# Kernel tuning notes

Measured on AMD Instinct MI355X. Metric: run time of the kernel, lower is better.

Reference implementation:

```python
import jax, jax.numpy as jnp
import numpy as np

N = 100000      # nodes
E = 3200000     # edges (avg degree 32)
F_IN = 500      # input features
HID = 8         # per-head hidden dim (layer 1)
HEADS = 8       # heads (layer 1)
NC = 41         # num classes (layer 2, 1 head)


def setup_inputs() -> dict:
    key = jax.random.key(0)
    ks = jax.random.split(key, 8)
    x = jax.random.normal(ks[0], (N, F_IN), jnp.float32)
    edge_index = jax.random.randint(ks[1], (2, E), 0, N, dtype=jnp.int64)
    W1 = jax.random.normal(ks[2], (F_IN, HEADS * HID), jnp.float32) / np.sqrt(F_IN)
    a1_src = jax.random.normal(ks[3], (HEADS, HID), jnp.float32) / np.sqrt(HID)
    a1_dst = jax.random.normal(ks[4], (HEADS, HID), jnp.float32) / np.sqrt(HID)
    W2 = jax.random.normal(ks[5], (HEADS * HID, NC), jnp.float32) / np.sqrt(HEADS * HID)
    a2_src = jax.random.normal(ks[6], (1, NC), jnp.float32) / np.sqrt(NC)
    a2_dst = jax.random.normal(ks[7], (1, NC), jnp.float32) / np.sqrt(NC)
    return {"x": x, "edge_index": edge_index, "W1": W1, "a1_src": a1_src,
            "a1_dst": a1_dst, "W2": W2, "a2_src": a2_src, "a2_dst": a2_dst}


def gat_layer(x, edge_index, W, a_src, a_dst, heads, out_dim, concat):
    n = x.shape[0]
    h = (x @ W).reshape(n, heads, out_dim)                    # [N,H,D]
    # per-node attention halves (avoids gathering full features for logits)
    alpha_src = jnp.einsum('nhd,hd->nh', h, a_src)            # [N,H]
    alpha_dst = jnp.einsum('nhd,hd->nh', h, a_dst)            # [N,H]
    src, dst = edge_index[0], edge_index[1]
    e = jax.nn.leaky_relu(alpha_src[src] + alpha_dst[dst], 0.2)  # [E,H]
    # segment softmax over incoming edges of each destination node
    e_max = jax.lax.stop_gradient(jax.ops.segment_max(e, dst, num_segments=n))
    e_exp = jnp.exp(e - e_max[dst])
    denom = jax.ops.segment_sum(e_exp, dst, num_segments=n)
    alpha = e_exp / (denom[dst] + 1e-16)                      # [E,H]
    msg = alpha[:, :, None] * h[src]                          # [E,H,D]
    out = jax.ops.segment_sum(msg, dst, num_segments=n)       # [N,H,D]
    return out.reshape(n, heads * out_dim) if concat else out.mean(axis=1)


def reference(x, edge_index, W1, a1_src, a1_dst, W2, a2_src, a2_dst):
    # dropout layers are identity at inference
    h = gat_layer(x, edge_index, W1, a1_src, a1_dst, HEADS, HID, True)   # [N,64]
    h = jax.nn.elu(h)
    out = gat_layer(h, edge_index, W2, a2_src, a2_dst, 1, NC, False)     # [N,41]
    return jax.nn.log_softmax(out, axis=1)
```

## Files before the change

kernel.cpp:

```cpp
#include <hip/hip_runtime.h>
#include <hip/hip_bf16.h>
#include <math.h>


#define DEV __device__ __forceinline__

constexpr int N_NODES = 100000;
constexpr int N_EDGES = 3200000;
constexpr int F_IN    = 500;
constexpr int HEADS   = 8;
constexpr int HID     = 8;
constexpr int D1      = HEADS * HID;
constexpr int NC      = 41;

constexpr int NB    = 196;
constexpr int BCAP  = 20480;
constexpr int SEPT  = 16;
constexpr int SCHUNK = 256 * SEPT;

constexpr int GROWS = 32;
constexpr int LROW  = 520;

constexpr int WSTR = 68;

typedef __attribute__((ext_vector_type(8))) short bf16x8;
typedef __attribute__((ext_vector_type(4))) float f32x4;

DEV float bf2f(unsigned short u) {
    return __uint_as_float(((unsigned int)u) << 16);
}
DEV unsigned short f2b(float f) {
    unsigned int u = __float_as_uint(f);
    unsigned int r = (u + 0x7FFFu + ((u >> 16) & 1u)) >> 16;
    return (unsigned short)r;
}
DEV float leaky(float e) { return e > 0.f ? e : 0.2f * e; }
DEV float readlane_f(float v, int l) {
    return __uint_as_float((unsigned int)__builtin_amdgcn_readlane((int)__float_as_uint(v), l));
}

__global__ void k_detect(const void* xraw, const void* eraw, int* flags) {
    const int lane = threadIdx.x & 63;
    const unsigned short* xu = (const unsigned short*)xraw;
    unsigned short v = xu[2 * lane];
    int e = (v >> 7) & 0xFF;
    int valid = (e == 0 || (e >= 90 && e <= 150)) ? 1 : 0;
    unsigned long long vm = __ballot(valid);
    const unsigned int* eu = (const unsigned int*)eraw;
    unsigned long long zm = __ballot(eu[2 * lane + 1] == 0u);
    if (lane == 0) {
        flags[0] = (__popcll(vm) < 56) ? 1 : 0;
        flags[1] = (__popcll(zm) == 64) ? 1 : 0;
    }
}

__global__ __launch_bounds__(256) void k_convert(const void* w1, const void* a1s, const void* a1d,
                                                 const void* w2, const void* a2s, const void* a2d,
                                                 const int* flags,
                                                 unsigned short* W1frag, float* A1Sf, float* A1Df,
                                                 float* W2f, float* A2Sf, float* A2Df) {
    const bool f32 = flags[0] != 0;
    if (blockIdx.x == 0) {
        auto conv = [&](const void* src, float* dst, int n) {
            if (f32) {
                const float* s = (const float*)src;
                for (int i = threadIdx.x; i < n; i += blockDim.x) dst[i] = s[i];
            } else {
                const unsigned short* s = (const unsigned short*)src;
                for (int i = threadIdx.x; i < n; i += blockDim.x) dst[i] = bf2f(s[i]);
            }
        };
        conv(a1s, A1Sf, HEADS * HID);
        conv(a1d, A1Df, HEADS * HID);
        conv(w2, W2f, D1 * NC);
        conv(a2s, A2Sf, NC);
        conv(a2d, A2Df, NC);
    }
    for (int idx = blockIdx.x * 256 + threadIdx.x; idx < 4 * 16 * 64 * 8; idx += 64 * 256) {
        int wid = idx >> 13, kb = (idx >> 9) & 15, ln = (idx >> 3) & 63, j = idx & 7;
        int k = kb * 32 + (ln >> 4) * 8 + j;
        int n = wid * 16 + (ln & 15);
        unsigned short bits = 0;
        if (k < F_IN) {
            if (f32) bits = f2b(((const float*)w1)[k * D1 + n]);
            else     bits = ((const unsigned short*)w1)[k * D1 + n];
        }
        W1frag[idx] = bits;
    }
}

__global__ __launch_bounds__(256) void k_bucket_scatter(const void* eraw, const int* flags,
                                                        int* bucket_cnt, unsigned int* staging) {
    __shared__ int bh[NB];
    const int t = threadIdx.x;
    for (int i = t; i < NB; i += 256) bh[i] = 0;
    __syncthreads();
    const bool e64 = flags[1] != 0;
    const unsigned int* eu = (const unsigned int*)eraw;
    const int e0 = blockIdx.x * SCHUNK;
    int sv[SEPT], dv[SEPT];
#pragma unroll
    for (int k = 0; k < SEPT; k++) {
        int i = e0 + k * 256 + t;
        if (i < N_EDGES) {
            if (e64) { sv[k] = (int)eu[2 * i]; dv[k] = (int)eu[2 * (N_EDGES + i)]; }
            else     { sv[k] = (int)eu[i];     dv[k] = (int)eu[N_EDGES + i]; }
            atomicAdd(&bh[dv[k] >> 9], 1);
        } else dv[k] = -1;
    }
    __syncthreads();
    for (int i = t; i < NB; i += 256) {
        int c = bh[i];
        int base = c ? atomicAdd(&bucket_cnt[i], c) : 0;
        bh[i] = i * BCAP + base;
    }
    __syncthreads();
#pragma unroll
    for (int k = 0; k < SEPT; k++) {
        if (dv[k] >= 0) {
            int b = dv[k] >> 9;
            int slot = atomicAdd(&bh[b], 1);
            staging[slot] = (unsigned)sv[k] | ((unsigned)(dv[k] & 511) << 17);
        }
    }
}

__global__ void k_cscan(const int* bucket_cnt, int* cbase, int* off) {
    __shared__ int s[256];
    int t = threadIdx.x;
    s[t] = (t < NB) ? bucket_cnt[t] : 0;
    __syncthreads();
    for (int o = 1; o < 256; o <<= 1) {
        int v = (t >= o) ? s[t - o] : 0;
        __syncthreads();
        s[t] += v;
        __syncthreads();
    }
    if (t < NB) cbase[t + 1] = s[t];
    if (t == 0) { cbase[0] = 0; off[N_NODES] = N_EDGES; }
}

__global__ __launch_bounds__(512) void k_csr_build(const unsigned int* __restrict__ staging,
                                                   const int* __restrict__ bucket_cnt,
                                                   const int* __restrict__ cbase,
                                                   int* __restrict__ off, int* __restrict__ csr) {
    __shared__ int sdeg[512];
    __shared__ int scur[512];
    const int t = threadIdx.x;
    const int b = blockIdx.x;
    const int n0 = b << 9;
    const int start = b * BCAP;
    const int end = start + bucket_cnt[b];
    const int base = cbase[b];
    sdeg[t] = 0;
    __syncthreads();
    for (int i = start + t; i < end; i += 512)
        atomicAdd(&sdeg[staging[i] >> 17], 1);
    __syncthreads();
    int d = sdeg[t];
    for (int o = 1; o < 512; o <<= 1) {
        int v = (t >= o) ? sdeg[t - o] : 0;
        __syncthreads();
        sdeg[t] += v;
        __syncthreads();
    }
    int excl = sdeg[t] - d;
    if (n0 + t < N_NODES) off[n0 + t] = base + excl;
    scur[t] = base + excl;
    __syncthreads();
    for (int i = start + t; i < end; i += 512) {
        unsigned v = staging[i];
        int slot = atomicAdd(&scur[v >> 17], 1);
        csr[slot] = (int)(v & 0x1FFFFu);
    }
}

__global__ __launch_bounds__(512, 8) void k_gemm1(const void* xraw, const int* flags,
                                                  const unsigned short* __restrict__ W1frag,
                                                  const float* A1Sf, const float* A1Df,
                                                  unsigned short* __restrict__ h1b,
                                                  float* __restrict__ as1,
                                                  float* __restrict__ ad1) {
    __shared__ unsigned short ldsx[GROWS * LROW];
    const int t = threadIdx.x;
    const int r0 = blockIdx.x * GROWS;
    const bool xf32 = flags[0] != 0;
#pragma unroll 4
    for (int it = 0; it < 8; it++) {
        int s = it * 512 + t;
        int row = s >> 7, c4 = s & 127;
        int row_g = r0 + row;
        ushort4 v = make_ushort4(0, 0, 0, 0);
        if (c4 < 125) {
            if (xf32) {
                float4 f = *(const float4*)((const float*)xraw + (size_t)row_g * F_IN + c4 * 4);
                v = make_ushort4(f2b(f.x), f2b(f.y), f2b(f.z), f2b(f.w));
            } else {
                v = *(const ushort4*)((const unsigned short*)xraw + (size_t)row_g * F_IN + c4 * 4);
            }
        }
        *(ushort4*)(ldsx + row * LROW + c4 * 4) = v;
    }
    __syncthreads();

    const int lane = t & 63;
    const int w = t >> 6;
    const int wid = __builtin_amdgcn_readfirstlane(w & 3);
    const int mb  = __builtin_amdgcn_readfirstlane(w >> 2);
    const int m = lane & 15, q = lane >> 4;
    f32x4 acc = {0.f, 0.f, 0.f, 0.f};
    const unsigned short* wf = W1frag + (size_t)wid * 8192;
    const unsigned short* arow = ldsx + (mb * 16 + m) * LROW + q * 8;
#pragma unroll 4
    for (int kb = 0; kb < 16; kb++) {
        bf16x8 b = *(const bf16x8*)(wf + (kb * 64 + lane) * 8);
        bf16x8 a = *(const bf16x8*)(arow + kb * 32);
        acc = __builtin_amdgcn_mfma_f32_16x16x32_bf16(a, b, acc, 0, 0, 0);
    }
    const int col = wid * 16 + m;
    const float a_s = A1Sf[col], a_d = A1Df[col];
    const int h = 2 * wid + (m >> 3);
#pragma unroll
    for (int reg = 0; reg < 4; reg++) {
        int gr = r0 + mb * 16 + q * 4 + reg;
        float vacc = acc[reg];
        h1b[(size_t)gr * D1 + col] = f2b(vacc);
        float ts = vacc * a_s, td = vacc * a_d;
        ts += __shfl_xor(ts, 1, 64); td += __shfl_xor(td, 1, 64);
        ts += __shfl_xor(ts, 2, 64); td += __shfl_xor(td, 2, 64);
        ts += __shfl_xor(ts, 4, 64); td += __shfl_xor(td, 4, 64);
        if ((lane & 7) == 0) {
            as1[gr * HEADS + h] = ts;
            ad1[gr * HEADS + h] = td;
        }
    }
}

__global__ __launch_bounds__(256) void k_agg1(const int* __restrict__ csr,
                                              const int* __restrict__ off,
                                              const unsigned short* __restrict__ h1b,
                                              const float* __restrict__ as1,
                                              const float* __restrict__ ad1,
                                              float* __restrict__ h1e) {
    __shared__ float wlds[4][8 * WSTR];
    const int t = threadIdx.x;
    const int lane = t & 63;
    const int n = (blockIdx.x * blockDim.x + t) >> 6;
    if (n >= N_NODES) return;
    const int beg = off[n], end = off[n + 1];
    const int h0 = lane >> 3;
    float* wl = wlds[(t >> 6) & 3];
    const float* wrow = wl + h0 * WSTR;
    const float* adp = ad1 + n * HEADS;
    float acc = 0.f, dsum = 0.f;
    for (int base = beg; base < end; base += 64) {
        const int cnt = min(64, end - base);
        int sl = 0;
        if (lane < cnt) {
            sl = csr[base + lane];
            const float* ap = as1 + sl * HEADS;
            float4 aa = *(const float4*)(ap);
            float4 ab = *(const float4*)(ap + 4);
            wl[0 * WSTR + lane] = __expf(leaky(aa.x + adp[0]));
            wl[1 * WSTR + lane] = __expf(leaky(aa.y + adp[1]));
            wl[2 * WSTR + lane] = __expf(leaky(aa.z + adp[2]));
            wl[3 * WSTR + lane] = __expf(leaky(aa.w + adp[3]));
            wl[4 * WSTR + lane] = __expf(leaky(ab.x + adp[4]));
            wl[5 * WSTR + lane] = __expf(leaky(ab.y + adp[5]));
            wl[6 * WSTR + lane] = __expf(leaky(ab.z + adp[6]));
            wl[7 * WSTR + lane] = __expf(leaky(ab.w + adp[7]));
        }
        asm volatile("s_waitcnt lgkmcnt(0)" ::: "memory");
        int j = 0;
        for (; j + 4 <= cnt; j += 4) {
            int s0 = __builtin_amdgcn_readlane(sl, j);
            int s1 = __builtin_amdgcn_readlane(sl, j + 1);
            int s2 = __builtin_amdgcn_readlane(sl, j + 2);
            int s3 = __builtin_amdgcn_readlane(sl, j + 3);
            float4 wv = *(const float4*)(wrow + j);
            float g0 = bf2f(h1b[(size_t)s0 * D1 + lane]);
            float g1 = bf2f(h1b[(size_t)s1 * D1 + lane]);
            float g2 = bf2f(h1b[(size_t)s2 * D1 + lane]);
            float g3 = bf2f(h1b[(size_t)s3 * D1 + lane]);
            acc = fmaf(wv.x, g0, acc); dsum += wv.x;
            acc = fmaf(wv.y, g1, acc); dsum += wv.y;
            acc = fmaf(wv.z, g2, acc); dsum += wv.z;
            acc = fmaf(wv.w, g3, acc); dsum += wv.w;
        }
        for (; j < cnt; j++) {
            int s = __builtin_amdgcn_readlane(sl, j);
            float w = wrow[j];
            acc = fmaf(w, bf2f(h1b[(size_t)s * D1 + lane]), acc);
            dsum += w;
        }
    }
    float v = acc / (dsum + 1e-16f);
    float o = v > 0.f ? v : (__expf(v) - 1.f);
    h1e[(size_t)n * D1 + lane] = o;
}

__global__ __launch_bounds__(256) void k_gemm2(const float* __restrict__ h1e,
                                               const float* __restrict__ W2f,
                                               const float* __restrict__ A2Sf,
                                               const float* __restrict__ A2Df,
                                               unsigned short* __restrict__ h2b,
                                               float* __restrict__ as2,
                                               float* __restrict__ ad2) {
    const int row = blockIdx.x * blockDim.x + threadIdx.x;
    if (row >= N_NODES) return;
    float acc[NC];
#pragma unroll
    for (int c = 0; c < NC; c++) acc[c] = 0.f;
    const float* xr = h1e + (size_t)row * D1;
    for (int k = 0; k < D1; k += 4) {
        float4 hv = *(const float4*)(xr + k);
#pragma unroll
        for (int c = 0; c < NC; c++) {
            acc[c] = fmaf(hv.x, W2f[(k + 0) * NC + c], acc[c]);
            acc[c] = fmaf(hv.y, W2f[(k + 1) * NC + c], acc[c]);
            acc[c] = fmaf(hv.z, W2f[(k + 2) * NC + c], acc[c]);
            acc[c] = fmaf(hv.w, W2f[(k + 3) * NC + c], acc[c]);
        }
    }
    float ts = 0.f, td = 0.f;
#pragma unroll
    for (int c = 0; c < NC; c++) {
        h2b[(size_t)row * NC + c] = f2b(acc[c]);
        ts = fmaf(acc[c], A2Sf[c], ts);
        td = fmaf(acc[c], A2Df[c], td);
    }
    as2[row] = ts;
    ad2[row] = td;
}

__global__ __launch_bounds__(256) void k_agg2(const int* __restrict__ csr,
                                              const int* __restrict__ off,
                                              const unsigned short* __restrict__ h2b,
                                              const float* __restrict__ as2,
                                              const float* __restrict__ ad2,
                                              const int* flags, void* out) {
    const int lane = threadIdx.x & 63;
    const int n = (blockIdx.x * blockDim.x + threadIdx.x) >> 6;
    if (n >= N_NODES) return;
    const int beg = off[n], end = off[n + 1];
    const float ad = ad2[n];
    const bool act = lane < NC;
    const int cl = act ? lane : 0;
    float acc = 0.f, dsum = 0.f;
    for (int base = beg; base < end; base += 64) {
        const int cnt = min(64, end - base);
        int idx = min(base + lane, N_EDGES - 1);
        int sl = csr[idx];
        float w = __expf(leaky(as2[sl] + ad));
        int j = 0;
        for (; j + 4 <= cnt; j += 4) {
            int s0 = __builtin_amdgcn_readlane(sl, j);
            int s1 = __builtin_amdgcn_readlane(sl, j + 1);
            int s2 = __builtin_amdgcn_readlane(sl, j + 2);
            int s3 = __builtin_amdgcn_readlane(sl, j + 3);
            float w0 = readlane_f(w, j);
            float w1 = readlane_f(w, j + 1);
            float w2 = readlane_f(w, j + 2);
            float w3 = readlane_f(w, j + 3);
            float g0 = bf2f(h2b[(size_t)s0 * NC + cl]);
            float g1 = bf2f(h2b[(size_t)s1 * NC + cl]);
            float g2 = bf2f(h2b[(size_t)s2 * NC + cl]);
            float g3 = bf2f(h2b[(size_t)s3 * NC + cl]);
            acc = fmaf(w0, g0, acc); dsum += w0;
            acc = fmaf(w1, g1, acc); dsum += w1;
            acc = fmaf(w2, g2, acc); dsum += w2;
            acc = fmaf(w3, g3, acc); dsum += w3;
        }
        for (; j < cnt; j++) {
            int s = __builtin_amdgcn_readlane(sl, j);
            float wj = readlane_f(w, j);
            acc = fmaf(wj, bf2f(h2b[(size_t)s * NC + cl]), acc);
            dsum += wj;
        }
    }
    float val = acc / (dsum + 1e-16f);
    float v = act ? val : -INFINITY;
    float m = v;
#pragma unroll
    for (int o = 1; o < 64; o <<= 1) m = fmaxf(m, __shfl_xor(m, o, 64));
    float ex = act ? __expf(val - m) : 0.f;
#pragma unroll
    for (int o = 1; o < 64; o <<= 1) ex += __shfl_xor(ex, o, 64);
    float res = val - m - __logf(ex);
    if (act) {
        if (flags[0])
            ((float*)out)[(size_t)n * NC + lane] = res;
        else
            ((__hip_bfloat16*)out)[(size_t)n * NC + lane] = __float2bfloat16(res);
    }
}

extern "C" void kernel_launch(void* const* d_in, const int* in_sizes, int n_in,
                              void* d_out, int out_size, void* d_ws, size_t ws_size,
                              hipStream_t stream) {
    char* p = (char*)d_ws;
    auto alloc = [&](size_t bytes) -> void* {
        void* r = (void*)p;
        p += (bytes + 255) & ~(size_t)255;
        return r;
    };
    int* flags  = (int*)alloc(16);
    unsigned short* W1frag = (unsigned short*)alloc(4 * 16 * 64 * 8 * 2);
    float* A1Sf = (float*)alloc(HEADS * HID * 4);
    float* A1Df = (float*)alloc(HEADS * HID * 4);
    float* W2f  = (float*)alloc((size_t)D1 * NC * 4);
    float* A2Sf = (float*)alloc(NC * 4);
    float* A2Df = (float*)alloc(NC * 4);
    unsigned short* h1b = (unsigned short*)alloc((size_t)N_NODES * D1 * 2);
    float* as1  = (float*)alloc((size_t)N_NODES * HEADS * 4);
    float* ad1  = (float*)alloc((size_t)N_NODES * HEADS * 4);
    float* h1e  = (float*)alloc((size_t)N_NODES * D1 * 4);
    unsigned short* h2b = (unsigned short*)alloc((size_t)N_NODES * NC * 2);
    float* as2  = (float*)alloc((size_t)N_NODES * 4);
    float* ad2  = (float*)alloc((size_t)N_NODES * 4);
    int* off    = (int*)alloc((size_t)(N_NODES + 1) * 4);
    int* csr    = (int*)alloc((size_t)N_EDGES * 4);
    int* bucket_cnt = (int*)alloc((size_t)NB * 4);
    int* cbase      = (int*)alloc((size_t)(NB + 1) * 4);
    unsigned int* staging = (unsigned int*)h1e;

    hipMemsetAsync(bucket_cnt, 0, (size_t)NB * 4, stream);

    k_detect<<<1, 64, 0, stream>>>(d_in[0], d_in[1], flags);
    k_convert<<<64, 256, 0, stream>>>(d_in[2], d_in[3], d_in[4], d_in[5], d_in[6], d_in[7],
                                      flags, W1frag, A1Sf, A1Df, W2f, A2Sf, A2Df);
    k_bucket_scatter<<<(N_EDGES + SCHUNK - 1) / SCHUNK, 256, 0, stream>>>(d_in[1], flags, bucket_cnt, staging);
    k_cscan<<<1, 256, 0, stream>>>(bucket_cnt, cbase, off);
    k_csr_build<<<NB, 512, 0, stream>>>(staging, bucket_cnt, cbase, off, csr);

    k_gemm1<<<(N_NODES + GROWS - 1) / GROWS, 512, 0, stream>>>(d_in[0], flags, W1frag, A1Sf, A1Df, h1b, as1, ad1);
    k_agg1<<<25000, 256, 0, stream>>>(csr, off, h1b, as1, ad1, h1e);
    k_gemm2<<<391, 256, 0, stream>>>(h1e, W2f, A2Sf, A2Df, h2b, as2, ad2);
    k_agg2<<<25000, 256, 0, stream>>>(csr, off, h2b, as2, ad2, flags, d_out);
}
```

Measured before the change: 614.5 us.

## Split GAT aggregation by head and class slab for cache-local gathers

Stores the layer-1 features, attention scores and ELU output head-major, and the layer-2 features in four 11-class slabs. Aggregation becomes persistent kernels where each block works on a single head or slab, so the random neighbour gathers stay inside a small table that can remain cache-resident. The cost is that CSR offsets and indices are reread once per head or slab, and each edge gather is narrower. Log-softmax moves into its own kernel that reads aggregated values from a scratch buffer.

```diff
diff --git a/kernel.cpp b/kernel.cpp
--- a/kernel.cpp
+++ b/kernel.cpp
@@ -12,6 +12,7 @@
 constexpr int HID     = 8;
 constexpr int D1      = HEADS * HID;
 constexpr int NC      = 41;
+constexpr int CW      = 11;
 
 constexpr int NB    = 196;
 constexpr int BCAP  = 20480;
@@ -21,8 +22,6 @@
 constexpr int GROWS = 32;
 constexpr int LROW  = 520;
 
-constexpr int WSTR = 68;
-
 typedef __attribute__((ext_vector_type(8))) short bf16x8;
 typedef __attribute__((ext_vector_type(4))) float f32x4;
 
@@ -35,9 +34,6 @@
     return (unsigned short)r;
 }
 DEV float leaky(float e) { return e > 0.f ? e : 0.2f * e; }
-DEV float readlane_f(float v, int l) {
-    return __uint_as_float((unsigned int)__builtin_amdgcn_readlane((int)__float_as_uint(v), l));
-}
 
 __global__ void k_detect(const void* xraw, const void* eraw, int* flags) {
     const int lane = threadIdx.x & 63;
@@ -178,9 +174,9 @@
 __global__ __launch_bounds__(512, 8) void k_gemm1(const void* xraw, const int* flags,
                                                   const unsigned short* __restrict__ W1frag,
                                                   const float* A1Sf, const float* A1Df,
-                                                  unsigned short* __restrict__ h1b,
-                                                  float* __restrict__ as1,
-                                                  float* __restrict__ ad1) {
+                                                  unsigned short* __restrict__ h1T,
+                                                  float* __restrict__ as1T,
+                                                  float* __restrict__ ad1T) {
     __shared__ unsigned short ldsx[GROWS * LROW];
     const int t = threadIdx.x;
     const int r0 = blockIdx.x * GROWS;
@@ -220,90 +216,76 @@
     const int col = wid * 16 + m;
     const float a_s = A1Sf[col], a_d = A1Df[col];
     const int h = 2 * wid + (m >> 3);
+    const int f = m & 7;
+    unsigned short* hslab = h1T + (size_t)h * (N_NODES * 8);
 #pragma unroll
     for (int reg = 0; reg < 4; reg++) {
         int gr = r0 + mb * 16 + q * 4 + reg;
         float vacc = acc[reg];
-        h1b[(size_t)gr * D1 + col] = f2b(vacc);
+        hslab[(size_t)gr * 8 + f] = f2b(vacc);
         float ts = vacc * a_s, td = vacc * a_d;
         ts += __shfl_xor(ts, 1, 64); td += __shfl_xor(td, 1, 64);
         ts += __shfl_xor(ts, 2, 64); td += __shfl_xor(td, 2, 64);
         ts += __shfl_xor(ts, 4, 64); td += __shfl_xor(td, 4, 64);
         if ((lane & 7) == 0) {
-            as1[gr * HEADS + h] = ts;
-            ad1[gr * HEADS + h] = td;
-        }
-    }
-}
-
-__global__ __launch_bounds__(256) void k_agg1(const int* __restrict__ csr,
-                                              const int* __restrict__ off,
-                                              const unsigned short* __restrict__ h1b,
-                                              const float* __restrict__ as1,
-                                              const float* __restrict__ ad1,
-                                              float* __restrict__ h1e) {
-    __shared__ float wlds[4][8 * WSTR];
+            as1T[(size_t)h * N_NODES + gr] = ts;
+            ad1T[(size_t)h * N_NODES + gr] = td;
+        }
+    }
+}
+
+__global__ __launch_bounds__(256) void k_agg1s(const int* __restrict__ csr,
+                                               const int* __restrict__ off,
+                                               const unsigned short* __restrict__ h1T,
+                                               const float* __restrict__ as1T,
+                                               const float* __restrict__ ad1T,
+                                               float* __restrict__ h1eT) {
     const int t = threadIdx.x;
     const int lane = t & 63;
-    const int n = (blockIdx.x * blockDim.x + t) >> 6;
-    if (n >= N_NODES) return;
-    const int beg = off[n], end = off[n + 1];
-    const int h0 = lane >> 3;
-    float* wl = wlds[(t >> 6) & 3];
-    const float* wrow = wl + h0 * WSTR;
-    const float* adp = ad1 + n * HEADS;
-    float acc = 0.f, dsum = 0.f;
-    for (int base = beg; base < end; base += 64) {
-        const int cnt = min(64, end - base);
-        int sl = 0;
-        if (lane < cnt) {
-            sl = csr[base + lane];
-            const float* ap = as1 + sl * HEADS;
-            float4 aa = *(const float4*)(ap);
-            float4 ab = *(const float4*)(ap + 4);
-            wl[0 * WSTR + lane] = __expf(leaky(aa.x + adp[0]));
-            wl[1 * WSTR + lane] = __expf(leaky(aa.y + adp[1]));
-            wl[2 * WSTR + lane] = __expf(leaky(aa.z + adp[2]));
-            wl[3 * WSTR + lane] = __expf(leaky(aa.w + adp[3]));
-            wl[4 * WSTR + lane] = __expf(leaky(ab.x + adp[4]));
-            wl[5 * WSTR + lane] = __expf(leaky(ab.y + adp[5]));
-            wl[6 * WSTR + lane] = __expf(leaky(ab.z + adp[6]));
-            wl[7 * WSTR + lane] = __expf(leaky(ab.w + adp[7]));
-        }
-        asm volatile("s_waitcnt lgkmcnt(0)" ::: "memory");
-        int j = 0;
-        for (; j + 4 <= cnt; j += 4) {
-            int s0 = __builtin_amdgcn_readlane(sl, j);
-            int s1 = __builtin_amdgcn_readlane(sl, j + 1);
-            int s2 = __builtin_amdgcn_readlane(sl, j + 2);
-            int s3 = __builtin_amdgcn_readlane(sl, j + 3);
-            float4 wv = *(const float4*)(wrow + j);
-            float g0 = bf2f(h1b[(size_t)s0 * D1 + lane]);
-            float g1 = bf2f(h1b[(size_t)s1 * D1 + lane]);
-            float g2 = bf2f(h1b[(size_t)s2 * D1 + lane]);
-            float g3 = bf2f(h1b[(size_t)s3 * D1 + lane]);
-            acc = fmaf(wv.x, g0, acc); dsum += wv.x;
-            acc = fmaf(wv.y, g1, acc); dsum += wv.y;
-            acc = fmaf(wv.z, g2, acc); dsum += wv.z;
-            acc = fmaf(wv.w, g3, acc); dsum += wv.w;
-        }
-        for (; j < cnt; j++) {
-            int s = __builtin_amdgcn_readlane(sl, j);
-            float w = wrow[j];
-            acc = fmaf(w, bf2f(h1b[(size_t)s * D1 + lane]), acc);
-            dsum += w;
-        }
-    }
-    float v = acc / (dsum + 1e-16f);
-    float o = v > 0.f ? v : (__expf(v) - 1.f);
-    h1e[(size_t)n * D1 + lane] = o;
-}
-
-__global__ __launch_bounds__(256) void k_gemm2(const float* __restrict__ h1e,
+    const int hp = blockIdx.x & 7;
+    const int w0 = ((blockIdx.x >> 3) << 2) + (t >> 6);
+    const int e = lane >> 3, f = lane & 7;
+    const unsigned short* tab = h1T + (size_t)hp * (N_NODES * 8);
+    const float* asl = as1T + (size_t)hp * N_NODES;
+    const float* adl = ad1T + (size_t)hp * N_NODES;
+    float* outs = h1eT + (size_t)hp * (N_NODES * 8);
+    for (int n = w0; n < N_NODES; n += 1024) {
+        const int beg = off[n], end = off[n + 1];
+        float acc = 0.f, dsum = 0.f;
+        if (beg < end) {
+            const float ad = adl[n];
+            for (int base = beg; base < end; base += 64) {
+                const int cnt = min(64, end - base);
+                int sl = csr[min(base + lane, end - 1)];
+                float wr = __expf(leaky(asl[sl] + ad));
+                float wv = (lane < cnt) ? wr : 0.f;
+                const int nr = (cnt + 7) >> 3;
+                for (int r = 0; r < nr; r++) {
+                    int ei = r * 8 + e;
+                    int se = __shfl(sl, ei, 64);
+                    float wb = __shfl(wv, ei, 64);
+                    float g = bf2f(tab[(size_t)se * 8 + f]);
+                    acc = fmaf(wb, g, acc);
+                    dsum += wb;
+                }
+            }
+#pragma unroll
+            for (int o = 8; o < 64; o <<= 1) {
+                acc += __shfl_xor(acc, o, 64);
+                dsum += __shfl_xor(dsum, o, 64);
+            }
+        }
+        float v = acc / (dsum + 1e-16f);
+        float oo = v > 0.f ? v : (__expf(v) - 1.f);
+        if (lane < 8) outs[(size_t)n * 8 + f] = oo;
+    }
+}
+
+__global__ __launch_bounds__(256) void k_gemm2(const float* __restrict__ h1eT,
                                                const float* __restrict__ W2f,
                                                const float* __restrict__ A2Sf,
                                                const float* __restrict__ A2Df,
-                                               unsigned short* __restrict__ h2b,
+                                               unsigned short* __restrict__ h2T,
                                                float* __restrict__ as2,
                                                float* __restrict__ ad2) {
     const int row = blockIdx.x * blockDim.x + threadIdx.x;
@@ -311,21 +293,28 @@
     float acc[NC];
 #pragma unroll
     for (int c = 0; c < NC; c++) acc[c] = 0.f;
-    const float* xr = h1e + (size_t)row * D1;
-    for (int k = 0; k < D1; k += 4) {
-        float4 hv = *(const float4*)(xr + k);
+#pragma unroll
+    for (int s8 = 0; s8 < 8; s8++) {
+        const float* xr = h1eT + (size_t)s8 * (N_NODES * 8) + (size_t)row * 8;
+        float4 ha = *(const float4*)(xr);
+        float4 hb = *(const float4*)(xr + 4);
+        const int k = s8 * 8;
 #pragma unroll
         for (int c = 0; c < NC; c++) {
-            acc[c] = fmaf(hv.x, W2f[(k + 0) * NC + c], acc[c]);
-            acc[c] = fmaf(hv.y, W2f[(k + 1) * NC + c], acc[c]);
-            acc[c] = fmaf(hv.z, W2f[(k + 2) * NC + c], acc[c]);
-            acc[c] = fmaf(hv.w, W2f[(k + 3) * NC + c], acc[c]);
+            acc[c] = fmaf(ha.x, W2f[(k + 0) * NC + c], acc[c]);
+            acc[c] = fmaf(ha.y, W2f[(k + 1) * NC + c], acc[c]);
+            acc[c] = fmaf(ha.z, W2f[(k + 2) * NC + c], acc[c]);
+            acc[c] = fmaf(ha.w, W2f[(k + 3) * NC + c], acc[c]);
+            acc[c] = fmaf(hb.x, W2f[(k + 4) * NC + c], acc[c]);
+            acc[c] = fmaf(hb.y, W2f[(k + 5) * NC + c], acc[c]);
+            acc[c] = fmaf(hb.z, W2f[(k + 6) * NC + c], acc[c]);
+            acc[c] = fmaf(hb.w, W2f[(k + 7) * NC + c], acc[c]);
         }
     }
     float ts = 0.f, td = 0.f;
 #pragma unroll
     for (int c = 0; c < NC; c++) {
-        h2b[(size_t)row * NC + c] = f2b(acc[c]);
+        h2T[(size_t)(c / CW) * (N_NODES * CW) + (size_t)row * CW + (c % CW)] = f2b(acc[c]);
         ts = fmaf(acc[c], A2Sf[c], ts);
         td = fmaf(acc[c], A2Df[c], td);
     }
@@ -333,65 +322,70 @@
     ad2[row] = td;
 }
 
-__global__ __launch_bounds__(256) void k_agg2(const int* __restrict__ csr,
-                                              const int* __restrict__ off,
-                                              const unsigned short* __restrict__ h2b,
-                                              const float* __restrict__ as2,
-                                              const float* __restrict__ ad2,
-                                              const int* flags, void* out) {
-    const int lane = threadIdx.x & 63;
-    const int n = (blockIdx.x * blockDim.x + threadIdx.x) >> 6;
-    if (n >= N_NODES) return;
-    const int beg = off[n], end = off[n + 1];
-    const float ad = ad2[n];
+__global__ __launch_bounds__(256) void k_agg2s(const int* __restrict__ csr,
+                                               const int* __restrict__ off,
+                                               const unsigned short* __restrict__ h2T,
+                                               const float* __restrict__ as2,
+                                               const float* __restrict__ ad2,
+                                               float* __restrict__ vals) {
+    const int t = threadIdx.x;
+    const int lane = t & 63;
+    const int p = blockIdx.x & 3;
+    const int w0 = ((blockIdx.x >> 2) << 2) + (t >> 6);
+    const int e = lane >> 4, c = lane & 15;
+    const int cc = c < CW ? c : 0;
+    const unsigned short* tab = h2T + (size_t)p * (N_NODES * CW);
+    for (int n = w0; n < N_NODES; n += 2048) {
+        const int beg = off[n], end = off[n + 1];
+        float acc = 0.f, dsum = 0.f;
+        if (beg < end) {
+            const float ad = ad2[n];
+            for (int base = beg; base < end; base += 64) {
+                const int cnt = min(64, end - base);
+                int sl = csr[min(base + lane, end - 1)];
+                float wr = __expf(leaky(as2[sl] + ad));
+                float wv = (lane < cnt) ? wr : 0.f;
+                const int nr = (cnt + 3) >> 2;
+                for (int r = 0; r < nr; r++) {
+                    int ei = r * 4 + e;
+                    int se = __shfl(sl, ei, 64);
+                    float wb = __shfl(wv, ei, 64);
+                    float g = bf2f(tab[(size_t)se * CW + cc]);
+                    acc = fmaf(wb, g, acc);
+                    dsum += wb;
+                }
+            }
+#pragma unroll
+            for (int o = 16; o < 64; o <<= 1) {
+                acc += __shfl_xor(acc, o, 64);
+                dsum += __shfl_xor(dsum, o, 64);
+            }
+        }
+        float v = acc / (dsum + 1e-16f);
+        if (lane < CW) vals[(size_t)n * 44 + p * CW + lane] = v;
+    }
+}
+
+__global__ __launch_bounds__(256) void k_lsm(const float* __restrict__ vals,
+                                             const int* flags, void* out) {
+    const int t = threadIdx.x;
+    const int lane = t & 63;
     const bool act = lane < NC;
-    const int cl = act ? lane : 0;
-    float acc = 0.f, dsum = 0.f;
-    for (int base = beg; base < end; base += 64) {
-        const int cnt = min(64, end - base);
-        int idx = min(base + lane, N_EDGES - 1);
-        int sl = csr[idx];
-        float w = __expf(leaky(as2[sl] + ad));
-        int j = 0;
-        for (; j + 4 <= cnt; j += 4) {
-            int s0 = __builtin_amdgcn_readlane(sl, j);
-            int s1 = __builtin_amdgcn_readlane(sl, j + 1);
-            int s2 = __builtin_amdgcn_readlane(sl, j + 2);
-            int s3 = __builtin_amdgcn_readlane(sl, j + 3);
-            float w0 = readlane_f(w, j);
-            float w1 = readlane_f(w, j + 1);
-            float w2 = readlane_f(w, j + 2);
-            float w3 = readlane_f(w, j + 3);
-            float g0 = bf2f(h2b[(size_t)s0 * NC + cl]);
-            float g1 = bf2f(h2b[(size_t)s1 * NC + cl]);
-            float g2 = bf2f(h2b[(size_t)s2 * NC + cl]);
-            float g3 = bf2f(h2b[(size_t)s3 * NC + cl]);
-            acc = fmaf(w0, g0, acc); dsum += w0;
-            acc = fmaf(w1, g1, acc); dsum += w1;
-            acc = fmaf(w2, g2, acc); dsum += w2;
-            acc = fmaf(w3, g3, acc); dsum += w3;
-        }
-        for (; j < cnt; j++) {
-            int s = __builtin_amdgcn_readlane(sl, j);
-            float wj = readlane_f(w, j);
-            acc = fmaf(wj, bf2f(h2b[(size_t)s * NC + cl]), acc);
-            dsum += wj;
-        }
-    }
-    float val = acc / (dsum + 1e-16f);
-    float v = act ? val : -INFINITY;
-    float m = v;
-#pragma unroll
-    for (int o = 1; o < 64; o <<= 1) m = fmaxf(m, __shfl_xor(m, o, 64));
-    float ex = act ? __expf(val - m) : 0.f;
-#pragma unroll
-    for (int o = 1; o < 64; o <<= 1) ex += __shfl_xor(ex, o, 64);
-    float res = val - m - __logf(ex);
-    if (act) {
-        if (flags[0])
-            ((float*)out)[(size_t)n * NC + lane] = res;
-        else
-            ((__hip_bfloat16*)out)[(size_t)n * NC + lane] = __float2bfloat16(res);
+    const int f32o = flags[0];
+    for (int n = blockIdx.x * 4 + (t >> 6); n < N_NODES; n += 4096) {
+        float val = act ? vals[(size_t)n * 44 + lane] : 0.f;
+        float v = act ? val : -INFINITY;
+        float m = v;
+#pragma unroll
+        for (int o = 1; o < 64; o <<= 1) m = fmaxf(m, __shfl_xor(m, o, 64));
+        float ex = act ? __expf(val - m) : 0.f;
+#pragma unroll
+        for (int o = 1; o < 64; o <<= 1) ex += __shfl_xor(ex, o, 64);
+        float res = val - m - __logf(ex);
+        if (act) {
+            if (f32o) ((float*)out)[(size_t)n * NC + lane] = res;
+            else      ((__hip_bfloat16*)out)[(size_t)n * NC + lane] = __float2bfloat16(res);
+        }
     }
 }
 
@@ -411,18 +405,19 @@
     float* W2f  = (float*)alloc((size_t)D1 * NC * 4);
     float* A2Sf = (float*)alloc(NC * 4);
     float* A2Df = (float*)alloc(NC * 4);
-    unsigned short* h1b = (unsigned short*)alloc((size_t)N_NODES * D1 * 2);
-    float* as1  = (float*)alloc((size_t)N_NODES * HEADS * 4);
-    float* ad1  = (float*)alloc((size_t)N_NODES * HEADS * 4);
-    float* h1e  = (float*)alloc((size_t)N_NODES * D1 * 4);
-    unsigned short* h2b = (unsigned short*)alloc((size_t)N_NODES * NC * 2);
+    unsigned short* h1T = (unsigned short*)alloc((size_t)N_NODES * D1 * 2);
+    float* as1T = (float*)alloc((size_t)HEADS * N_NODES * 4);
+    float* ad1T = (float*)alloc((size_t)HEADS * N_NODES * 4);
+    float* h1eT = (float*)alloc((size_t)HEADS * N_NODES * 8 * 4);
+    unsigned short* h2T = (unsigned short*)alloc((size_t)4 * N_NODES * CW * 2 + 64);
     float* as2  = (float*)alloc((size_t)N_NODES * 4);
     float* ad2  = (float*)alloc((size_t)N_NODES * 4);
     int* off    = (int*)alloc((size_t)(N_NODES + 1) * 4);
     int* csr    = (int*)alloc((size_t)N_EDGES * 4);
     int* bucket_cnt = (int*)alloc((size_t)NB * 4);
     int* cbase      = (int*)alloc((size_t)(NB + 1) * 4);
-    unsigned int* staging = (unsigned int*)h1e;
+    unsigned int* staging = (unsigned int*)h1eT;
+    float* vals = (float*)h1eT;
 
     hipMemsetAsync(bucket_cnt, 0, (size_t)NB * 4, stream);
 
@@ -433,8 +428,9 @@
     k_cscan<<<1, 256, 0, stream>>>(bucket_cnt, cbase, off);
     k_csr_build<<<NB, 512, 0, stream>>>(staging, bucket_cnt, cbase, off, csr);
 
-    k_gemm1<<<(N_NODES + GROWS - 1) / GROWS, 512, 0, stream>>>(d_in[0], flags, W1frag, A1Sf, A1Df, h1b, as1, ad1);
-    k_agg1<<<25000, 256, 0, stream>>>(csr, off, h1b, as1, ad1, h1e);
-    k_gemm2<<<391, 256, 0, stream>>>(h1e, W2f, A2Sf, A2Df, h2b, as2, ad2);
-    k_agg2<<<25000, 256, 0, stream>>>(csr, off, h2b, as2, ad2, flags, d_out);
-}
+    k_gemm1<<<(N_NODES + GROWS - 1) / GROWS, 512, 0, stream>>>(d_in[0], flags, W1frag, A1Sf, A1Df, h1T, as1T, ad1T);
+    k_agg1s<<<2048, 256, 0, stream>>>(csr, off, h1T, as1T, ad1T, h1eT);
+    k_gemm2<<<391, 256, 0, stream>>>(h1eT, W2f, A2Sf, A2Df, h2T, as2, ad2);
+    k_agg2s<<<2048, 256, 0, stream>>>(csr, off, h2T, as2, ad2, vals);
+    k_lsm<<<1024, 256, 0, stream>>>(vals, flags, d_out);
+}
```

Measured after the change: 894.3 us. +45.5%, slower.

## Fuse edge bucket scatter with first GEMM in one launch; pad h2 rows

Applied to the files above, without the earlier changes.

The edge bucket-scatter work and the layer-1 GEMM are merged into one kernel. The first blocks scatter edges and the remaining blocks run the GEMM, so the two independent phases share one grid and can run at the same time. The scatter now uses 512 threads per block with 8 edges per thread and reuses the GEMM's LDS buffer for its histogram. Separately, the layer-2 features are stored with a 64-element row stride instead of 41, to align the gathers in the second aggregation at the cost of extra memory.

```diff
diff --git a/kernel.cpp b/kernel.cpp
--- a/kernel.cpp
+++ b/kernel.cpp
@@ -12,14 +12,17 @@
 constexpr int HID     = 8;
 constexpr int D1      = HEADS * HID;
 constexpr int NC      = 41;
+constexpr int NCP     = 64;
 
 constexpr int NB    = 196;
 constexpr int BCAP  = 20480;
-constexpr int SEPT  = 16;
-constexpr int SCHUNK = 256 * SEPT;
+constexpr int SEPT  = 8;
+constexpr int SCHUNK = 512 * SEPT;
+constexpr int SBLKS = (N_EDGES + SCHUNK - 1) / SCHUNK;
 
 constexpr int GROWS = 32;
 constexpr int LROW  = 520;
+constexpr int GBLKS = N_NODES / GROWS;
 
 constexpr int WSTR = 68;
 
@@ -89,38 +92,101 @@
     }
 }
 
-__global__ __launch_bounds__(256) void k_bucket_scatter(const void* eraw, const int* flags,
-                                                        int* bucket_cnt, unsigned int* staging) {
-    __shared__ int bh[NB];
+__global__ __launch_bounds__(512, 8) void k_gemm1_scat(const void* xraw, const void* eraw,
+                                                       const int* flags,
+                                                       const unsigned short* __restrict__ W1frag,
+                                                       const float* A1Sf, const float* A1Df,
+                                                       unsigned short* __restrict__ h1b,
+                                                       float* __restrict__ as1,
+                                                       float* __restrict__ ad1,
+                                                       int* bucket_cnt, unsigned int* staging) {
+    __shared__ unsigned short ldsx[GROWS * LROW];
     const int t = threadIdx.x;
-    for (int i = t; i < NB; i += 256) bh[i] = 0;
+
+    if (blockIdx.x < SBLKS) {
+        int* bh = (int*)ldsx;
+        for (int i = t; i < NB; i += 512) bh[i] = 0;
+        __syncthreads();
+        const bool e64 = flags[1] != 0;
+        const unsigned int* eu = (const unsigned int*)eraw;
+        const int e0 = blockIdx.x * SCHUNK;
+        int sv[SEPT], dv[SEPT];
+#pragma unroll
+        for (int k = 0; k < SEPT; k++) {
+            int i = e0 + k * 512 + t;
+            if (i < N_EDGES) {
+                if (e64) { sv[k] = (int)eu[2 * i]; dv[k] = (int)eu[2 * (N_EDGES + i)]; }
+                else     { sv[k] = (int)eu[i];     dv[k] = (int)eu[N_EDGES + i]; }
+                atomicAdd(&bh[dv[k] >> 9], 1);
+            } else dv[k] = -1;
+        }
+        __syncthreads();
+        for (int i = t; i < NB; i += 512) {
+            int c = bh[i];
+            int base = c ? atomicAdd(&bucket_cnt[i], c) : 0;
+            bh[i] = i * BCAP + base;
+        }
+        __syncthreads();
+#pragma unroll
+        for (int k = 0; k < SEPT; k++) {
+            if (dv[k] >= 0) {
+                int b = dv[k] >> 9;
+                int slot = atomicAdd(&bh[b], 1);
+                staging[slot] = (unsigned)sv[k] | ((unsigned)(dv[k] & 511) << 17);
+            }
+        }
+        return;
+    }
+
+    const int r0 = (blockIdx.x - SBLKS) * GROWS;
+    const bool xf32 = flags[0] != 0;
+#pragma unroll 4
+    for (int it = 0; it < 8; it++) {
+        int s = it * 512 + t;
+        int row = s >> 7, c4 = s & 127;
+        int row_g = r0 + row;
+        ushort4 v = make_ushort4(0, 0, 0, 0);
+        if (c4 < 125) {
+            if (xf32) {
+                float4 f = *(const float4*)((const float*)xraw + (size_t)row_g * F_IN + c4 * 4);
+                v = make_ushort4(f2b(f.x), f2b(f.y), f2b(f.z), f2b(f.w));
+            } else {
+                v = *(const ushort4*)((const unsigned short*)xraw + (size_t)row_g * F_IN + c4 * 4);
+            }
+        }
+        *(ushort4*)(ldsx + row * LROW + c4 * 4) = v;
+    }
     __syncthreads();
-    const bool e64 = flags[1] != 0;
-    const unsigned int* eu = (const unsigned int*)eraw;
-    const int e0 = blockIdx.x * SCHUNK;
-    int sv[SEPT], dv[SEPT];
-#pragma unroll
-    for (int k = 0; k < SEPT; k++) {
-        int i = e0 + k * 256 + t;
-        if (i < N_EDGES) {
-            if (e64) { sv[k] = (int)eu[2 * i]; dv[k] = (int)eu[2 * (N_EDGES + i)]; }
-            else     { sv[k] = (int)eu[i];     dv[k] = (int)eu[N_EDGES + i]; }
-            atomicAdd(&bh[dv[k] >> 9], 1);
-        } else dv[k] = -1;
-    }
-    __syncthreads();
-    for (int i = t; i < NB; i += 256) {
-        int c = bh[i];
-        int base = c ? atomicAdd(&bucket_cnt[i], c) : 0;
-        bh[i] = i * BCAP + base;
-    }
-    __syncthreads();
-#pragma unroll
-    for (int k = 0; k < SEPT; k++) {
-        if (dv[k] >= 0) {
-            int b = dv[k] >> 9;
-            int slot = atomicAdd(&bh[b], 1);
-            staging[slot] = (unsigned)sv[k] | ((unsigned)(dv[k] & 511) << 17);
+
+    const int lane = t & 63;
+    const int w = t >> 6;
+    const int wid = __builtin_amdgcn_readfirstlane(w & 3);
+    const int mb  = __builtin_amdgcn_readfirstlane(w >> 2);
+    const int m = lane & 15, q = lane >> 4;
+    f32x4 acc = {0.f, 0.f, 0.f, 0.f};
+    const unsigned short* wf = W1frag + (size_t)wid * 8192;
+    const unsigned short* arow = ldsx + (mb * 16 + m) * LROW + q * 8;
+#pragma unroll 4
+    for (int kb = 0; kb < 16; kb++) {
+        bf16x8 b = *(const bf16x8*)(wf + (kb * 64 + lane) * 8);
+        bf16x8 a = *(const bf16x8*)(arow + kb * 32);
+        acc = __builtin_amdgcn_mfma_f32_16x16x32_bf16(a, b, acc, 0, 0, 0);
+    }
+    const int col = wid * 16 + m;
+    const float a_s = A1Sf[col], a_d = A1Df[col];
+    const int h = 2 * wid + (m >> 3);
+#pragma unroll
+    for (int reg = 0; reg < 4; reg++) {
+        int gr = r0 + mb * 16 + q * 4 + reg;
+        float vacc = acc[reg];
+        h1b[(size_t)gr * D1 + col] = f2b(vacc);
+        float ts = vacc * a_s, td = vacc * a_d;
+        ts += __shfl_xor(ts, 1, 64); td += __shfl_xor(td, 1, 64);
+        ts += __shfl_xor(ts, 2, 64); td += __shfl_xor(td, 2, 64);
+        ts += __shfl_xor(ts, 4, 64); td += __shfl_xor(td, 4, 64);
+        if ((lane & 7) == 0) {
+            as1[gr * HEADS + h] = ts;
+            ad1[gr * HEADS + h] = td;
         }
     }
 }
@@ -172,67 +238,6 @@
         unsigned v = staging[i];
         int slot = atomicAdd(&scur[v >> 17], 1);
         csr[slot] = (int)(v & 0x1FFFFu);
-    }
-}
-
-__global__ __launch_bounds__(512, 8) void k_gemm1(const void* xraw, const int* flags,
-                                                  const unsigned short* __restrict__ W1frag,
-                                                  const float* A1Sf, const float* A1Df,
-                                                  unsigned short* __restrict__ h1b,
-                                                  float* __restrict__ as1,
-                                                  float* __restrict__ ad1) {
-    __shared__ unsigned short ldsx[GROWS * LROW];
-    const int t = threadIdx.x;
-    const int r0 = blockIdx.x * GROWS;
-    const bool xf32 = flags[0] != 0;
-#pragma unroll 4
-    for (int it = 0; it < 8; it++) {
-        int s = it * 512 + t;
-        int row = s >> 7, c4 = s & 127;
-        int row_g = r0 + row;
-        ushort4 v = make_ushort4(0, 0, 0, 0);
-        if (c4 < 125) {
-            if (xf32) {
-                float4 f = *(const float4*)((const float*)xraw + (size_t)row_g * F_IN + c4 * 4);
-                v = make_ushort4(f2b(f.x), f2b(f.y), f2b(f.z), f2b(f.w));
-            } else {
-                v = *(const ushort4*)((const unsigned short*)xraw + (size_t)row_g * F_IN + c4 * 4);
-            }
-        }
-        *(ushort4*)(ldsx + row * LROW + c4 * 4) = v;
-    }
-    __syncthreads();
-
-    const int lane = t & 63;
-    const int w = t >> 6;
-    const int wid = __builtin_amdgcn_readfirstlane(w & 3);
-    const int mb  = __builtin_amdgcn_readfirstlane(w >> 2);
-    const int m = lane & 15, q = lane >> 4;
-    f32x4 acc = {0.f, 0.f, 0.f, 0.f};
-    const unsigned short* wf = W1frag + (size_t)wid * 8192;
-    const unsigned short* arow = ldsx + (mb * 16 + m) * LROW + q * 8;
-#pragma unroll 4
-    for (int kb = 0; kb < 16; kb++) {
-        bf16x8 b = *(const bf16x8*)(wf + (kb * 64 + lane) * 8);
-        bf16x8 a = *(const bf16x8*)(arow + kb * 32);
-        acc = __builtin_amdgcn_mfma_f32_16x16x32_bf16(a, b, acc, 0, 0, 0);
-    }
-    const int col = wid * 16 + m;
-    const float a_s = A1Sf[col], a_d = A1Df[col];
-    const int h = 2 * wid + (m >> 3);
-#pragma unroll
-    for (int reg = 0; reg < 4; reg++) {
-        int gr = r0 + mb * 16 + q * 4 + reg;
-        float vacc = acc[reg];
-        h1b[(size_t)gr * D1 + col] = f2b(vacc);
-        float ts = vacc * a_s, td = vacc * a_d;
-        ts += __shfl_xor(ts, 1, 64); td += __shfl_xor(td, 1, 64);
-        ts += __shfl_xor(ts, 2, 64); td += __shfl_xor(td, 2, 64);
-        ts += __shfl_xor(ts, 4, 64); td += __shfl_xor(td, 4, 64);
-        if ((lane & 7) == 0) {
-            as1[gr * HEADS + h] = ts;
-            ad1[gr * HEADS + h] = td;
-        }
     }
 }
 
@@ -303,7 +308,7 @@
                                                const float* __restrict__ W2f,
                                                const float* __restrict__ A2Sf,
                                                const float* __restrict__ A2Df,
-                                               unsigned short* __restrict__ h2b,
+                                               unsigned short* __restrict__ h2p,
                                                float* __restrict__ as2,
                                                float* __restrict__ ad2) {
     const int row = blockIdx.x * blockDim.x + threadIdx.x;
@@ -325,7 +330,7 @@
     float ts = 0.f, td = 0.f;
 #pragma unroll
     for (int c = 0; c < NC; c++) {
-        h2b[(size_t)row * NC + c] = f2b(acc[c]);
+        h2p[(size_t)row * NCP + c] = f2b(acc[c]);
         ts = fmaf(acc[c], A2Sf[c], ts);
         td = fmaf(acc[c], A2Df[c], td);
     }
@@ -335,7 +340,7 @@
 
 __global__ __launch_bounds__(256) void k_agg2(const int* __restrict__ csr,
                                               const int* __restrict__ off,
-                                              const unsigned short* __restrict__ h2b,
+                                              const unsigned short* __restrict__ h2p,
                                               const float* __restrict__ as2,
                                               const float* __restrict__ ad2,
                                               const int* flags, void* out) {
@@ -362,10 +367,10 @@
             float w1 = readlane_f(w, j + 1);
             float w2 = readlane_f(w, j + 2);
             float w3 = readlane_f(w, j + 3);
-            float g0 = bf2f(h2b[(size_t)s0 * NC + cl]);
-            float g1 = bf2f(h2b[(size_t)s1 * NC + cl]);
-            float g2 = bf2f(h2b[(size_t)s2 * NC + cl]);
-            float g3 = bf2f(h2b[(size_t)s3 * NC + cl]);
+            float g0 = bf2f(h2p[(size_t)s0 * NCP + cl]);
+            float g1 = bf2f(h2p[(size_t)s1 * NCP + cl]);
+            float g2 = bf2f(h2p[(size_t)s2 * NCP + cl]);
+            float g3 = bf2f(h2p[(size_t)s3 * NCP + cl]);
             acc = fmaf(w0, g0, acc); dsum += w0;
             acc = fmaf(w1, g1, acc); dsum += w1;
             acc = fmaf(w2, g2, acc); dsum += w2;
@@ -374,7 +379,7 @@
         for (; j < cnt; j++) {
             int s = __builtin_amdgcn_readlane(sl, j);
             float wj = readlane_f(w, j);
-            acc = fmaf(wj, bf2f(h2b[(size_t)s * NC + cl]), acc);
+            acc = fmaf(wj, bf2f(h2p[(size_t)s * NCP + cl]), acc);
             dsum += wj;
         }
     }
@@ -415,7 +420,7 @@
     float* as1  = (float*)alloc((size_t)N_NODES * HEADS * 4);
     float* ad1  = (float*)alloc((size_t)N_NODES * HEADS * 4);
     float* h1e  = (float*)alloc((size_t)N_NODES * D1 * 4);
-    unsigned short* h2b = (unsigned short*)alloc((size_t)N_NODES * NC * 2);
+    unsigned short* h2p = (unsigned short*)alloc((size_t)N_NODES * NCP * 2);
     float* as2  = (float*)alloc((size_t)N_NODES * 4);
     float* ad2  = (float*)alloc((size_t)N_NODES * 4);
     int* off    = (int*)alloc((size_t)(N_NODES + 1) * 4);
@@ -429,12 +434,13 @@
     k_detect<<<1, 64, 0, stream>>>(d_in[0], d_in[1], flags);
     k_convert<<<64, 256, 0, stream>>>(d_in[2], d_in[3], d_in[4], d_in[5], d_in[6], d_in[7],
                                       flags, W1frag, A1Sf, A1Df, W2f, A2Sf, A2Df);
-    k_bucket_scatter<<<(N_EDGES + SCHUNK - 1) / SCHUNK, 256, 0, stream>>>(d_in[1], flags, bucket_cnt, staging);
+    k_gemm1_scat<<<SBLKS + GBLKS, 512, 0, stream>>>(d_in[0], d_in[1], flags, W1frag,
+                                                    A1Sf, A1Df, h1b, as1, ad1,
+                                                    bucket_cnt, staging);
     k_cscan<<<1, 256, 0, stream>>>(bucket_cnt, cbase, off);
     k_csr_build<<<NB, 512, 0, stream>>>(staging, bucket_cnt, cbase, off, csr);
 
-    k_gemm1<<<(N_NODES + GROWS - 1) / GROWS, 512, 0, stream>>>(d_in[0], flags, W1frag, A1Sf, A1Df, h1b, as1, ad1);
     k_agg1<<<25000, 256, 0, stream>>>(csr, off, h1b, as1, ad1, h1e);
-    k_gemm2<<<391, 256, 0, stream>>>(h1e, W2f, A2Sf, A2Df, h2b, as2, ad2);
-    k_agg2<<<25000, 256, 0, stream>>>(csr, off, h2b, as2, ad2, flags, d_out);
-}
+    k_gemm2<<<391, 256, 0, stream>>>(h1e, W2f, A2Sf, A2Df, h2p, as2, ad2);
+    k_agg2<<<25000, 256, 0, stream>>>(csr, off, h2p, as2, ad2, flags, d_out);
+}
```

Measured after the change: 603.6 us. About the same (-1.8%).
